# Kernel optimization log

Hardware: AMD Instinct MI355X
Metric: run time of the kernel (lower is better)

The kernel has to match this reference:

```python
import jax, jax.numpy as jnp
import numpy as np

V_MIN = -10.0
V_MAX = 10.0
NUM_ATOMS = 51
ATOM_DELTA = (V_MAX - V_MIN) / (NUM_ATOMS - 1)
BS = 1_000_000


def setup_inputs() -> dict:
    key = jax.random.key(0)
    k1, k2 = jax.random.split(key)
    reward = jax.random.normal(k1, (BS,), dtype=jnp.float32) * 3.0
    probs = jax.random.uniform(k2, (BS, NUM_ATOMS), dtype=jnp.float32)
    atom_values = (V_MIN + ATOM_DELTA * jnp.arange(NUM_ATOMS)).astype(jnp.float32)
    return {"reward": reward, "probs": probs, "atom_values": atom_values}


def reference(reward, probs, atom_values):
    # Categorical (C51) Bellman projection, expressed as a scatter-add
    # instead of the original's dense [bs, A, A] projection matrix + bmm.
    bs, A = probs.shape
    # shifted & clamped atom support: [bs, A]
    new_vals = jnp.clip(atom_values[None, :] + reward[:, None], V_MIN, V_MAX)
    idx = (new_vals - V_MIN) / ATOM_DELTA           # fractional atom index
    lower = jnp.floor(idx)
    upper = jnp.ceil(idx)
    same = lower == upper                           # idx landed exactly on an atom
    l_coef = jnp.where(same, 1.0, upper - idx)      # original sets 1.0 when l == u
    u_coef = idx - lower                            # 0 when same
    li = lower.astype(jnp.int32)
    ui = upper.astype(jnp.int32)
    rows = jnp.broadcast_to(jnp.arange(bs)[:, None], (bs, A))
    out = jnp.zeros_like(probs)
    out = out.at[rows, li].add(l_coef * probs)
    out = out.at[rows, ui].add(u_coef * probs)
    return out
```

## Files before the change

kernel.cpp:

```cpp
#include <hip/hip_runtime.h>

#define NA 51
#define ROWS 256

__global__ __launch_bounds__(256, 3) void c51_bellman_kernel(
    const float* __restrict__ reward,
    const float* __restrict__ probs,
    float* __restrict__ out,
    int bs)
{
    __shared__ float lds[ROWS * NA];
    const int tid   = threadIdx.x;
    const int row0  = blockIdx.x * ROWS;
    const int nrows = min(ROWS, bs - row0);
    const int nelem = nrows * NA;
    const int n4    = nelem >> 2;

    const float4* p4 = (const float4*)(probs + (size_t)row0 * NA);
    float4* l4 = (float4*)lds;
    for (int e4 = tid; e4 < n4; e4 += ROWS) l4[e4] = p4[e4];
    for (int e = (n4 << 2) + tid; e < nelem; e += ROWS)
        lds[e] = probs[(size_t)row0 * NA + e];
    __syncthreads();

    if (tid < nrows) {
        const float s  = reward[row0 + tid] * 2.5f;
        const float kf = floorf(s);
        const int   k  = (int)kf;
        const float f  = s - kf;
        const float* rp = lds + tid * NA;

        float m_lo = 0.0f, m_hi = 0.0f;
        #pragma unroll
        for (int j = 0; j < NA; ++j) {
            const float pj = rp[j];
            const float t  = (float)j + s;
            if (t < 0.0f)  m_lo += pj;
            if (t > 50.0f) m_hi += pj;
        }

        float o[NA];
        float prev;
        {
            const int jm = -k - 1;
            const int cm = min(max(jm, 0), NA - 1);
            const float v = rp[cm];
            prev = (jm >= 0 && jm < NA) ? v : 0.0f;
        }
        #pragma unroll
        for (int i = 0; i < NA; ++i) {
            const int j = i - k;
            const int c = min(max(j, 0), NA - 1);
            const float v = rp[c];
            const float cur = (j >= 0 && j < NA) ? v : 0.0f;
            const float w1 = ((float)i + f <= 50.0f) ? (1.0f - f) : 0.0f;
            const float w2 = ((float)(i - 1) + f >= 0.0f) ? f : 0.0f;
            o[i] = w1 * cur + w2 * prev;
            prev = cur;
        }
        o[0]      += m_lo;
        o[NA - 1] += m_hi;

        float* wp = lds + tid * NA;
        #pragma unroll
        for (int i = 0; i < NA; ++i) wp[i] = o[i];
    }
    __syncthreads();

    float4* o4 = (float4*)(out + (size_t)row0 * NA);
    const float4* l4c = (const float4*)lds;
    for (int e4 = tid; e4 < n4; e4 += ROWS) o4[e4] = l4c[e4];
    for (int e = (n4 << 2) + tid; e < nelem; e += ROWS)
        out[(size_t)row0 * NA + e] = lds[e];
}

extern "C" void kernel_launch(void* const* d_in, const int* in_sizes, int n_in,
                              void* d_out, int out_size, void* d_ws, size_t ws_size,
                              hipStream_t stream) {
    const float* reward = (const float*)d_in[0];
    const float* probs  = (const float*)d_in[1];
    float* out = (float*)d_out;
    const int bs = in_sizes[0];

    const int blocks = (bs + ROWS - 1) / ROWS;
    c51_bellman_kernel<<<blocks, ROWS, 0, stream>>>(reward, probs, out, bs);
}
```

Baseline: 365.5 us.

## Use single-wave blocks with direct global-to-LDS loads and guarded window reads

Shrinks blocks to 64 rows, which is one wavefront, so the __syncthreads barriers become waitcnt fences. Probabilities are staged with global_load_lds DMA straight into LDS. The shifted input is read as a contiguous 52-element window from an LDS buffer padded with guard regions, replacing per-element clamped indexing and branchy weights. Possible costs are more blocks with a smaller LDS footprint each, window reads that touch neighbouring rows or guard memory, and reliance on wave-synchronous LDS visibility.

New measurement: 344.7 us. 1.06x faster.

```diff
diff --git a/kernel.cpp b/kernel.cpp
--- a/kernel.cpp
+++ b/kernel.cpp
@@ -1,34 +1,56 @@
 #include <hip/hip_runtime.h>
 
 #define NA 51
-#define ROWS 256
+#define ROWS 64
+#define GUARD 56
+#define NDATA (ROWS * NA)
+#define KCLAMP 52
 
-__global__ __launch_bounds__(256, 3) void c51_bellman_kernel(
+__global__ __launch_bounds__(ROWS, 3) void c51_bellman_kernel(
     const float* __restrict__ reward,
     const float* __restrict__ probs,
     float* __restrict__ out,
     int bs)
 {
-    __shared__ float lds[ROWS * NA];
+    __shared__ float lds[GUARD + NDATA + GUARD];
+    float* data = lds + GUARD;
     const int tid   = threadIdx.x;
     const int row0  = blockIdx.x * ROWS;
     const int nrows = min(ROWS, bs - row0);
-    const int nelem = nrows * NA;
-    const int n4    = nelem >> 2;
 
-    const float4* p4 = (const float4*)(probs + (size_t)row0 * NA);
-    float4* l4 = (float4*)lds;
-    for (int e4 = tid; e4 < n4; e4 += ROWS) l4[e4] = p4[e4];
-    for (int e = (n4 << 2) + tid; e < nelem; e += ROWS)
-        lds[e] = probs[(size_t)row0 * NA + e];
-    __syncthreads();
+    float s = 0.0f;
+    if (tid < nrows) s = reward[row0 + tid] * 2.5f;
+
+    if (nrows == ROWS) {
+        const char* src = (const char*)(probs + (size_t)row0 * NA);
+        #pragma unroll
+        for (int t = 0; t < 12; ++t) {
+            __builtin_amdgcn_global_load_lds(
+                (const __attribute__((address_space(1))) void*)
+                    (unsigned long long)(src + t * 1024 + tid * 16),
+                (__attribute__((address_space(3))) void*)
+                    (unsigned long long)(data + t * 256),
+                16, 0, 0);
+        }
+        if (tid < 48) {
+            const float4 v = *(const float4*)(src + 12288 + (size_t)tid * 16);
+            *(float4*)(data + 3072 + tid * 4) = v;
+        }
+    } else {
+        const int nelem = nrows * NA;
+        for (int e = tid; e < nelem; e += ROWS)
+            data[e] = probs[(size_t)row0 * NA + e];
+    }
+    asm volatile("s_waitcnt vmcnt(0) lgkmcnt(0)" ::: "memory");
+    __builtin_amdgcn_sched_barrier(0);
 
     if (tid < nrows) {
-        const float s  = reward[row0 + tid] * 2.5f;
         const float kf = floorf(s);
-        const int   k  = (int)kf;
         const float f  = s - kf;
-        const float* rp = lds + tid * NA;
+        int k = (int)kf;
+        k = min(max(k, -KCLAMP), KCLAMP);
+
+        const float* rp = data + tid * NA;
 
         float m_lo = 0.0f, m_hi = 0.0f;
         #pragma unroll
@@ -39,39 +61,39 @@
             if (t > 50.0f) m_hi += pj;
         }
 
-        float o[NA];
-        float prev;
-        {
-            const int jm = -k - 1;
-            const int cm = min(max(jm, 0), NA - 1);
-            const float v = rp[cm];
-            prev = (jm >= 0 && jm < NA) ? v : 0.0f;
-        }
+        const float* wb = data + tid * NA - k - 1;
+        float w[52];
+        #pragma unroll
+        for (int m = 0; m < 52; ++m) w[m] = wb[m];
+
+        float* wp = data + tid * NA;
+        const float w1 = 1.0f - f;
+        float prev = ((unsigned)(-k - 1) <= 50u) ? w[0] : 0.0f;
         #pragma unroll
         for (int i = 0; i < NA; ++i) {
-            const int j = i - k;
-            const int c = min(max(j, 0), NA - 1);
-            const float v = rp[c];
-            const float cur = (j >= 0 && j < NA) ? v : 0.0f;
-            const float w1 = ((float)i + f <= 50.0f) ? (1.0f - f) : 0.0f;
-            const float w2 = ((float)(i - 1) + f >= 0.0f) ? f : 0.0f;
-            o[i] = w1 * cur + w2 * prev;
+            const float cur = ((unsigned)(i - k) <= 50u) ? w[i + 1] : 0.0f;
+            float o;
+            if (i == 0)           o = w1 * cur + m_lo;
+            else if (i == NA - 1) o = ((f == 0.0f) ? cur : f * prev) + m_hi;
+            else                  o = w1 * cur + f * prev;
+            wp[i] = o;
             prev = cur;
         }
-        o[0]      += m_lo;
-        o[NA - 1] += m_hi;
+    }
+    asm volatile("s_waitcnt lgkmcnt(0)" ::: "memory");
+    __builtin_amdgcn_sched_barrier(0);
 
-        float* wp = lds + tid * NA;
+    if (nrows == ROWS) {
+        float4* o4 = (float4*)(out + (size_t)row0 * NA);
+        const float4* l4 = (const float4*)data;
         #pragma unroll
-        for (int i = 0; i < NA; ++i) wp[i] = o[i];
+        for (int t = 0; t < 12; ++t) o4[t * 64 + tid] = l4[t * 64 + tid];
+        if (tid < 48) o4[768 + tid] = l4[768 + tid];
+    } else {
+        const int nelem = nrows * NA;
+        for (int e = tid; e < nelem; e += ROWS)
+            out[(size_t)row0 * NA + e] = data[e];
     }
-    __syncthreads();
-
-    float4* o4 = (float4*)(out + (size_t)row0 * NA);
-    const float4* l4c = (const float4*)lds;
-    for (int e4 = tid; e4 < n4; e4 += ROWS) o4[e4] = l4c[e4];
-    for (int e = (n4 << 2) + tid; e < nelem; e += ROWS)
-        out[(size_t)row0 * NA + e] = lds[e];
 }
 
 extern "C" void kernel_launch(void* const* d_in, const int* in_sizes, int n_in,
```
